# Performance work log

Measured on AMD Instinct MI355X. Metric: run time of the kernel, lower is better.

## Reference

```python
import jax, jax.numpy as jnp
import numpy as np

HEADS = 8
CHANNELS = 256
RR = 1
DH = CHANNELS // RR                 # per-head channels
ATT = HEADS * DH                    # 2048
# exact scale from the torch module
SCALE = (1.0 / np.sqrt(CHANNELS // RR)) / np.sqrt(2.0 / (CHANNELS + 3 * ATT)) * np.sqrt(2.0 / (CHANNELS + ATT))


def setup_inputs() -> dict:
    key = jax.random.key(0)
    k1, k2, k3, k4, k5 = jax.random.split(key, 5)
    x = jax.random.normal(k1, (8, CHANNELS, 32, 32), dtype=jnp.float32)
    # 1x1 conv weights stored as [out_ch, in_ch]
    w_in = jax.random.normal(k2, (3 * ATT, CHANNELS), dtype=jnp.float32) * (1.0 / np.sqrt(CHANNELS))
    b_in = jax.random.normal(k3, (3 * ATT,), dtype=jnp.float32) * 0.02
    w_out = jax.random.normal(k4, (CHANNELS, ATT), dtype=jnp.float32) * (1.0 / np.sqrt(ATT))
    b_out = jax.random.normal(k5, (CHANNELS,), dtype=jnp.float32) * 0.02
    return {"x": x, "w_in": w_in, "b_in": b_in, "w_out": w_out, "b_out": b_out}


def reference(x, w_in, b_in, w_out, b_out):
    n, c, h, w = x.shape
    L = h * w
    xf = x.reshape(n, c, L)
    # 1x1 conv in = channel-mixing matmul, then fixed scale
    scaled = (jnp.einsum('ncl,oc->nol', xf, w_in) + b_in[:, None]) * jnp.float32(SCALE)
    s = scaled.reshape(n, HEADS, 3 * DH, L)
    q, k, v = s[:, :, :DH], s[:, :, DH:2 * DH], s[:, :, 2 * DH:]   # each (n, H, DH, L)
    att = jnp.einsum('nhdl,nhdm->nhlm', q, k)                       # (n, H, L, L)
    # softmax over the FLATTENED L*L axis (global per head), as in the torch code
    att = jax.nn.softmax(att.reshape(n, HEADS, L * L), axis=2).reshape(n, HEADS, L, L)
    out = jnp.einsum('nhdl,nhlm->nhdm', v, att)                     # (n, H, DH, L)
    out = out.reshape(n, ATT, L)
    out = jnp.einsum('nal,ca->ncl', out, w_out) + b_out[:, None]
    return out.reshape(n, c, h, w)
```

## Files before the change

kernel.cpp:

```cpp
#include <hip/hip_runtime.h>
#include <hip/hip_bf16.h>


typedef __bf16 bf16x8 __attribute__((ext_vector_type(8)));
typedef __bf16 bf16x4 __attribute__((ext_vector_type(4)));
typedef float f32x4 __attribute__((ext_vector_type(4)));
typedef float f32x16 __attribute__((ext_vector_type(16)));
typedef __hip_bfloat16 bf16;

__device__ __forceinline__ void async_copy16(const void* g, void* s) {
    __builtin_amdgcn_global_load_lds(
        (const __attribute__((address_space(1))) unsigned int*)g,
        (__attribute__((address_space(3))) unsigned int*)s, 16, 0, 0);
}

__device__ __forceinline__ bf16x8 scale8(bf16x8 v, float s) {
    bf16x8 r;
#pragma unroll
    for (int e = 0; e < 8; ++e) r[e] = (__bf16)((float)v[e] * s);
    return r;
}

__global__ __launch_bounds__(256)
void gemm_nt(const bf16* __restrict__ A, const bf16* __restrict__ B, void* __restrict__ Cvoid,
             int M, int N, int K, int lda, int ldb, int ldc,
             long asn, long ash, long bsn, long bsh, long csn, long csh,
             int H, int mode, const float* __restrict__ bias, const float* __restrict__ Zp,
             float scale,
             bf16* __restrict__ outQ, bf16* __restrict__ outK, bf16* __restrict__ outV)
{
    __shared__ __align__(16) bf16 smem[17408];
    bf16* Alds = smem;
    bf16* Blds = smem + 8192;

    const int tid  = threadIdx.x;
    const int wave = tid >> 6;
    const int lane = tid & 63;
    const int z  = blockIdx.z;
    const int zn = z / H, zh = z % H;

    const bf16* Ab = A + zn * asn + zh * ash;
    const bf16* Bb = B + zn * bsn + zh * bsh;

    const long tM = (long)blockIdx.y * 128;
    const long tN = (long)blockIdx.x * 128;

    const int wr   = (wave >> 1) * 64;
    const int wc   = (wave & 1) * 64;
    const int l15  = lane & 15;
    const int quad = lane >> 4;

    f32x4 acc[4][4] = {};

    const int kiters = K >> 6;
    const bool regB = (mode == 4);

#pragma unroll
    for (int i = 0; i < 4; ++i) {
        const int flat = i * 256 + tid;
        const int row  = flat >> 3;
        const int kcs  = (flat & 7) ^ (row & 7);
        async_copy16(Ab + (tM + row) * (long)lda + kcs * 8,
                     (char*)Alds + (long)(i * 256 + wave * 64) * 16);
        if (!regB) {
            async_copy16(Bb + (tN + row) * (long)ldb + kcs * 8,
                         (char*)Blds + (long)(i * 256 + wave * 64) * 16);
        }
    }
    if (regB) {
        const float zi0 = 1.0f / Zp[zn * 8];
#pragma unroll
        for (int i = 0; i < 4; ++i) {
            const int flat = i * 256 + tid;
            const int row  = flat >> 3;
            const int kcs  = (flat & 7) ^ (row & 7);
            bf16x8 b = *(const bf16x8*)(Bb + (tN + row) * (long)ldb + kcs * 8);
            *(bf16x8*)((char*)Blds + (long)flat * 16) = scale8(b, zi0);
        }
    }

    bf16x8 pfA[4], pfB[4];
    for (int kt = 0; kt < kiters; ++kt) {
        __syncthreads();
        const bool has_next = (kt + 1 < kiters);
        float zin = 1.0f;
        if (has_next) {
            const long kof = (long)(kt + 1) * 64;
            if (regB) zin = 1.0f / Zp[zn * 8 + ((kt + 1) >> 2)];
#pragma unroll
            for (int i = 0; i < 4; ++i) {
                const int flat = i * 256 + tid;
                const int row  = flat >> 3;
                const int kcs  = (flat & 7) ^ (row & 7);
                pfA[i] = *(const bf16x8*)(Ab + (tM + row) * (long)lda + kof + kcs * 8);
                pfB[i] = *(const bf16x8*)(Bb + (tN + row) * (long)ldb + kof + kcs * 8);
            }
        }
#pragma unroll
        for (int kk = 0; kk < 2; ++kk) {
            bf16x8 af[4], bfv[4];
#pragma unroll
            for (int i = 0; i < 4; ++i) {
                const int r = wr + i * 16 + l15;
                af[i] = *(const bf16x8*)(Alds + r * 64 + ((kk * 4 + quad) ^ (r & 7)) * 8);
            }
#pragma unroll
            for (int j = 0; j < 4; ++j) {
                const int r = wc + j * 16 + l15;
                bfv[j] = *(const bf16x8*)(Blds + r * 64 + ((kk * 4 + quad) ^ (r & 7)) * 8);
            }
#pragma unroll
            for (int i = 0; i < 4; ++i)
#pragma unroll
                for (int j = 0; j < 4; ++j)
                    acc[i][j] = __builtin_amdgcn_mfma_f32_16x16x32_bf16(af[i], bfv[j], acc[i][j], 0, 0, 0);
        }
        if (has_next) {
            __builtin_amdgcn_sched_barrier(0);
            __builtin_amdgcn_s_barrier();
            __builtin_amdgcn_sched_barrier(0);
#pragma unroll
            for (int i = 0; i < 4; ++i) {
                const int flat = i * 256 + tid;
                *(bf16x8*)((char*)Alds + (long)flat * 16) = pfA[i];
                *(bf16x8*)((char*)Blds + (long)flat * 16) = regB ? scale8(pfB[i], zin) : pfB[i];
            }
        }
    }

    if (mode >= 3) {
        float* C = (float*)Cvoid + zn * csn + zh * csh;
#pragma unroll
        for (int i = 0; i < 4; ++i)
#pragma unroll
            for (int j = 0; j < 4; ++j)
#pragma unroll
                for (int r = 0; r < 4; ++r) {
                    const long row = tM + wr + i * 16 + quad * 4 + r;
                    const long col = tN + wc + j * 16 + l15;
                    C[row * (long)ldc + col] = acc[i][j][r] + bias[row];
                }
        return;
    }

    const int x    = blockIdx.x;
    const int part = x % 6;
    const int nh   = zn * 8 + x / 6;
    const int d0   = (part & 1) * 128;
    const int by   = blockIdx.y;

    __syncthreads();
    if (part < 4) {
#pragma unroll
        for (int i = 0; i < 4; ++i)
#pragma unroll
            for (int j = 0; j < 4; ++j)
#pragma unroll
                for (int r = 0; r < 4; ++r) {
                    const int row = wr + i * 16 + quad * 4 + r;
                    const int col = wc + j * 16 + l15;
                    const float v = (acc[i][j][r] + bias[tN + col]) * scale;
                    const int c32 = col >> 3;
                    const int slot = (c32 & 8) | ((c32 & 7) ^ (row & 7));
                    smem[row * 128 + slot * 8 + (col & 7)] = __float2bfloat16(v);
                }
        __syncthreads();
        bf16* dst = (part < 2) ? outQ : outK;
#pragma unroll
        for (int k = 0; k < 8; ++k) {
            const int flat = k * 256 + tid;
            const int seg  = flat >> 6, ln = flat & 63;
            const int lb   = seg >> 3, wloc = seg & 7;
            const int row  = lb * 32 + (ln & 31);
            const int c32  = wloc * 2 + (ln >> 5);
            const int slot = (c32 & 8) | ((c32 & 7) ^ (row & 7));
            const f32x4 val = *(const f32x4*)(smem + row * 128 + slot * 8);
            const long addr = ((long)(nh * 32 + by * 4 + lb) * 16 + (d0 >> 4) + wloc) * 512 + ln * 8;
            *(f32x4*)(dst + addr) = val;
        }
    } else {
#pragma unroll
        for (int i = 0; i < 4; ++i)
#pragma unroll
            for (int j = 0; j < 4; ++j)
#pragma unroll
                for (int r = 0; r < 4; ++r) {
                    const int row = wr + i * 16 + quad * 4 + r;
                    const int col = wc + j * 16 + l15;
                    const float v = (acc[i][j][r] + bias[tN + col]) * scale;
                    const int rc = row >> 3;
                    const int slotT = (rc & 8) | ((rc & 7) ^ (col & 7));
                    smem[col * 128 + slotT * 8 + (row & 7)] = __float2bfloat16(v);
                }
        __syncthreads();
#pragma unroll
        for (int k = 0; k < 8; ++k) {
            const int flat = k * 256 + tid;
            const int seg  = flat >> 6, ln = flat & 63;
            const int kwl  = seg >> 2, g2l = seg & 3;
            const int dl   = g2l * 32 + (ln & 31);
            const int lc   = kwl * 2 + (ln >> 5);
            const int slotT = (lc & 8) | ((lc & 7) ^ (dl & 7));
            const f32x4 val = *(const f32x4*)(smem + dl * 128 + slotT * 8);
            const long addr = ((long)(nh * 64 + by * 8 + kwl) * 8 + (d0 >> 5) + g2l) * 512 + ln * 8;
            *(f32x4*)(outV + addr) = val;
        }
    }
}

__global__ __launch_bounds__(256, 2)
void attn_fused(const bf16* __restrict__ Qsw, const bf16* __restrict__ Ksw,
                const bf16* __restrict__ Vsw, bf16* __restrict__ out_tt,
                float* __restrict__ Z)
{
    __shared__ __align__(16) bf16 smem[16904];
    bf16* Ps  = smem;
    float* Zs = (float*)(smem + 16896);

    const int tid  = threadIdx.x;
    const int wave = tid >> 6, lane = tid & 63;
    const int l31  = lane & 31, hw = lane >> 5;

    const int b   = blockIdx.x;
    const int xcd = b & 7, s = b >> 3;
    const int nh  = xcd * 8 + (s >> 4);
    const int mt  = s & 15;
    const int n   = nh >> 3, h = nh & 7;
    const long m0 = (long)mt * 64;

    const int wl = wave & 1, wm = wave >> 1;

    bf16x8 Kf[16];
    {
        const bf16* kb = Ksw + ((long)(nh * 32 + mt * 2 + wm) * 16) * 512 + lane * 8;
#pragma unroll
        for (int w = 0; w < 16; ++w)
            Kf[w] = *(const bf16x8*)(kb + w * 512);
    }

    f32x16 accO[2][2] = {};
    float zsum = 0.0f;

    for (int lt = 0; lt < 16; ++lt) {
        bf16x8 vf[4][2];
#pragma unroll
        for (int kw = 0; kw < 4; ++kw)
#pragma unroll
            for (int dt = 0; dt < 2; ++dt)
                vf[kw][dt] = *(const bf16x8*)(
                    Vsw + ((long)(nh * 64 + lt * 4 + kw) * 8 + wave * 2 + dt) * 512 + lane * 8);

        const bf16* qb = Qsw + ((long)(nh * 32 + lt * 2 + wl) * 16) * 512 + lane * 8;
        f32x16 a0 = {}, a1 = {};
#pragma unroll
        for (int w = 0; w < 16; w += 2) {
            const bf16x8 q0 = *(const bf16x8*)(qb + w * 512);
            a0 = __builtin_amdgcn_mfma_f32_32x32x16_bf16(q0, Kf[w], a0, 0, 0, 0);
            const bf16x8 q1 = *(const bf16x8*)(qb + (w + 1) * 512);
            a1 = __builtin_amdgcn_mfma_f32_32x32x16_bf16(q1, Kf[w + 1], a1, 0, 0, 0);
        }

#pragma unroll
        for (int g = 0; g < 4; ++g) {
            bf16x4 pk;
#pragma unroll
            for (int e = 0; e < 4; ++e) {
                const float v = __expf(a0[g * 4 + e] + a1[g * 4 + e]);
                zsum += v;
                pk[e] = (__bf16)v;
            }
            const int l  = wl * 32 + 4 * hw + 8 * g;
            const int kw = l >> 4, off = l & 15;
            *(bf16x4*)(Ps + kw * 1536 + (wm * 32 + l31) * 24 + off) = pk;
        }

        __syncthreads();

#pragma unroll
        for (int kw = 0; kw < 4; ++kw) {
            bf16x8 pf[2];
#pragma unroll
            for (int mh = 0; mh < 2; ++mh)
                pf[mh] = *(const bf16x8*)(Ps + kw * 1536 + (mh * 32 + l31) * 24 + hw * 8);
#pragma unroll
            for (int mh = 0; mh < 2; ++mh)
#pragma unroll
                for (int dt = 0; dt < 2; ++dt)
                    accO[mh][dt] = __builtin_amdgcn_mfma_f32_32x32x16_bf16(
                        pf[mh], vf[kw][dt], accO[mh][dt], 0, 0, 0);
        }
        __syncthreads();
    }

#pragma unroll
    for (int o = 32; o > 0; o >>= 1) zsum += __shfl_down(zsum, o);
    if (lane == 0) Zs[wave] = zsum;

    bf16* Cs = smem;
#pragma unroll
    for (int mh = 0; mh < 2; ++mh)
#pragma unroll
        for (int dt = 0; dt < 2; ++dt)
#pragma unroll
            for (int r = 0; r < 16; ++r) {
                const int m = mh * 32 + (r & 3) + 8 * (r >> 2) + 4 * hw;
                const int d = wave * 64 + dt * 32 + l31;
                Cs[m * 264 + d] = __float2bfloat16(accO[mh][dt][r]);
            }
    __syncthreads();
    if (tid == 0) atomicAdd(Z + nh, (Zs[0] + Zs[1]) + (Zs[2] + Zs[3]));

    bf16* Ob = out_tt + (long)n * 2097152 + m0 * 2048 + h * 256;
#pragma unroll
    for (int k = 0; k < 8; ++k) {
        const int flat = k * 256 + tid;
        const int row  = flat >> 5;
        const int c    = flat & 31;
        const f32x4 val = *(const f32x4*)((const char*)Cs + row * 528 + c * 16);
        *(f32x4*)((char*)(Ob + (long)row * 2048) + c * 16) = val;
    }
}

__global__ void prep_convert(const float* __restrict__ w_in, const float* __restrict__ w_out,
                             bf16* __restrict__ w_in_b, bf16* __restrict__ w_out_b,
                             float* __restrict__ Z)
{
    const long gid = (long)blockIdx.x * 256 + threadIdx.x;
    if (blockIdx.x == 0 && threadIdx.x < 64) Z[threadIdx.x] = 0.0f;
    const long n1 = 6144L * 256;
    const long n2 = 256L * 2048;
    const long stride = (long)gridDim.x * 256;
    for (long i = gid; i < n1; i += stride) w_in_b[i] = __float2bfloat16(w_in[i]);
    for (long i = gid; i < n2; i += stride) w_out_b[i] = __float2bfloat16(w_out[i]);
}

__global__ void prep_xt(const float* __restrict__ x, bf16* __restrict__ x_t)
{
    __shared__ float tile[64][65];
    const int b = blockIdx.x;
    const int n = blockIdx.y;
    const int ct = b & 3, lt = b >> 2;
    const int t = threadIdx.x;
    const float* xp = x + (long)n * 256 * 1024;
#pragma unroll
    for (int i = 0; i < 16; ++i) {
        const int flat = i * 256 + t;
        const int cl = flat >> 6, ll = flat & 63;
        tile[cl][ll] = xp[(long)(ct * 64 + cl) * 1024 + lt * 64 + ll];
    }
    __syncthreads();
    bf16* xo = x_t + (long)n * 1024 * 256;
#pragma unroll
    for (int i = 0; i < 16; ++i) {
        const int flat = i * 256 + t;
        const int lr = flat >> 6, cr = flat & 63;
        xo[(long)(lt * 64 + lr) * 256 + ct * 64 + cr] = __float2bfloat16(tile[cr][lr]);
    }
}

extern "C" void kernel_launch(void* const* d_in, const int* in_sizes, int n_in,
                              void* d_out, int out_size, void* d_ws, size_t ws_size,
                              hipStream_t stream)
{
    const float* x     = (const float*)d_in[0];
    const float* w_in  = (const float*)d_in[1];
    const float* b_in  = (const float*)d_in[2];
    const float* w_out = (const float*)d_in[3];
    const float* b_out = (const float*)d_in[4];
    float* out = (float*)d_out;

    const float SCALE = 0.10416666666666667f;

    char* p = (char*)d_ws;
    bf16* Qsw     = (bf16*)p;  p += 33554432;
    bf16* Ksw     = (bf16*)p;  p += 33554432;
    bf16* Vsw     = (bf16*)p;  p += 33554432;
    bf16* out_tt  = (bf16*)p;  p += 33554432;
    bf16* x_t     = (bf16*)p;  p += 4194304;
    bf16* w_in_b  = (bf16*)p;  p += 3145728;
    bf16* w_out_b = (bf16*)p;  p += 1048576;
    float* Z      = (float*)p; p += 256;

    prep_convert<<<2048, 256, 0, stream>>>(w_in, w_out, w_in_b, w_out_b, Z);
    prep_xt<<<dim3(64, 8), 256, 0, stream>>>(x, x_t);

    gemm_nt<<<dim3(48, 8, 8), 256, 0, stream>>>(
        x_t, w_in_b, nullptr,
        1024, 6144, 256, 256, 256, 0,
        1024L * 256, 0, 0, 0, 0, 0,
        1, 0, b_in, nullptr, SCALE, Qsw, Ksw, Vsw);

    attn_fused<<<1024, 256, 0, stream>>>(Qsw, Ksw, Vsw, out_tt, Z);

    gemm_nt<<<dim3(8, 2, 8), 256, 0, stream>>>(
        w_out_b, out_tt, out,
        256, 1024, 2048, 2048, 2048, 1024,
        0, 0, 1024L * 2048, 0, 256L * 1024, 0,
        1, 4, b_out, Z, 1.0f, nullptr, nullptr, nullptr);
}
```

Measured before the change: 245.8 us.

## Split-K output projection with atomics; double-buffer P and prefetch Q in attention

The output projection GEMM is split into two K halves (heads 0-3 and 4-7) across a doubled grid z-dimension. Partial sums are accumulated into the output with atomicAdd, so the output is zeroed in the prep kernel and the bias is added only by the first half. In the attention kernel, Q fragments are held in registers and prefetched for the next tile after the barrier, and the P tile in LDS is double-buffered so the second per-iteration __syncthreads can be dropped. This trades fp32 atomics and extra registers for more parallelism in the small final GEMM and fewer barriers in the attention loop.

```diff
diff --git a/kernel.cpp b/kernel.cpp
--- a/kernel.cpp
+++ b/kernel.cpp
@@ -68,7 +68,7 @@
         }
     }
     if (regB) {
-        const float zi0 = 1.0f / Zp[zn * 8];
+        const float zi0 = 1.0f / Zp[zn * 8 + zh * 4];
 #pragma unroll
         for (int i = 0; i < 4; ++i) {
             const int flat = i * 256 + tid;
@@ -86,7 +86,7 @@
         float zin = 1.0f;
         if (has_next) {
             const long kof = (long)(kt + 1) * 64;
-            if (regB) zin = 1.0f / Zp[zn * 8 + ((kt + 1) >> 2)];
+            if (regB) zin = 1.0f / Zp[zn * 8 + zh * 4 + ((kt + 1) >> 2)];
 #pragma unroll
             for (int i = 0; i < 4; ++i) {
                 const int flat = i * 256 + tid;
@@ -138,7 +138,12 @@
                 for (int r = 0; r < 4; ++r) {
                     const long row = tM + wr + i * 16 + quad * 4 + r;
                     const long col = tN + wc + j * 16 + l15;
-                    C[row * (long)ldc + col] = acc[i][j][r] + bias[row];
+                    if (mode == 4) {
+                        const float v = acc[i][j][r] + (zh == 0 ? bias[row] : 0.0f);
+                        atomicAdd(&C[row * (long)ldc + col], v);
+                    } else {
+                        C[row * (long)ldc + col] = acc[i][j][r] + bias[row];
+                    }
                 }
         return;
     }
@@ -237,6 +242,13 @@
         for (int w = 0; w < 16; ++w)
             Kf[w] = *(const bf16x8*)(kb + w * 512);
     }
+    bf16x8 Qc[16];
+    {
+        const bf16* qb = Qsw + ((long)(nh * 32 + wl) * 16) * 512 + lane * 8;
+#pragma unroll
+        for (int w = 0; w < 16; ++w)
+            Qc[w] = *(const bf16x8*)(qb + w * 512);
+    }
 
     f32x16 accO[2][2] = {};
     float zsum = 0.0f;
@@ -250,16 +262,14 @@
                 vf[kw][dt] = *(const bf16x8*)(
                     Vsw + ((long)(nh * 64 + lt * 4 + kw) * 8 + wave * 2 + dt) * 512 + lane * 8);
 
-        const bf16* qb = Qsw + ((long)(nh * 32 + lt * 2 + wl) * 16) * 512 + lane * 8;
         f32x16 a0 = {}, a1 = {};
 #pragma unroll
         for (int w = 0; w < 16; w += 2) {
-            const bf16x8 q0 = *(const bf16x8*)(qb + w * 512);
-            a0 = __builtin_amdgcn_mfma_f32_32x32x16_bf16(q0, Kf[w], a0, 0, 0, 0);
-            const bf16x8 q1 = *(const bf16x8*)(qb + (w + 1) * 512);
-            a1 = __builtin_amdgcn_mfma_f32_32x32x16_bf16(q1, Kf[w + 1], a1, 0, 0, 0);
-        }
-
+            a0 = __builtin_amdgcn_mfma_f32_32x32x16_bf16(Qc[w], Kf[w], a0, 0, 0, 0);
+            a1 = __builtin_amdgcn_mfma_f32_32x32x16_bf16(Qc[w + 1], Kf[w + 1], a1, 0, 0, 0);
+        }
+
+        bf16* Pb = Ps + (lt & 1) * 6144;
 #pragma unroll
         for (int g = 0; g < 4; ++g) {
             bf16x4 pk;
@@ -271,17 +281,24 @@
             }
             const int l  = wl * 32 + 4 * hw + 8 * g;
             const int kw = l >> 4, off = l & 15;
-            *(bf16x4*)(Ps + kw * 1536 + (wm * 32 + l31) * 24 + off) = pk;
+            *(bf16x4*)(Pb + kw * 1536 + (wm * 32 + l31) * 24 + off) = pk;
         }
 
         __syncthreads();
+
+        if (lt < 15) {
+            const bf16* qn = Qsw + ((long)(nh * 32 + (lt + 1) * 2 + wl) * 16) * 512 + lane * 8;
+#pragma unroll
+            for (int w = 0; w < 16; ++w)
+                Qc[w] = *(const bf16x8*)(qn + w * 512);
+        }
 
 #pragma unroll
         for (int kw = 0; kw < 4; ++kw) {
             bf16x8 pf[2];
 #pragma unroll
             for (int mh = 0; mh < 2; ++mh)
-                pf[mh] = *(const bf16x8*)(Ps + kw * 1536 + (mh * 32 + l31) * 24 + hw * 8);
+                pf[mh] = *(const bf16x8*)(Pb + kw * 1536 + (mh * 32 + l31) * 24 + hw * 8);
 #pragma unroll
             for (int mh = 0; mh < 2; ++mh)
 #pragma unroll
@@ -289,8 +306,9 @@
                     accO[mh][dt] = __builtin_amdgcn_mfma_f32_32x32x16_bf16(
                         pf[mh], vf[kw][dt], accO[mh][dt], 0, 0, 0);
         }
-        __syncthreads();
-    }
+    }
+
+    __syncthreads();
 
 #pragma unroll
     for (int o = 32; o > 0; o >>= 1) zsum += __shfl_down(zsum, o);
@@ -323,10 +341,12 @@
 
 __global__ void prep_convert(const float* __restrict__ w_in, const float* __restrict__ w_out,
                              bf16* __restrict__ w_in_b, bf16* __restrict__ w_out_b,
-                             float* __restrict__ Z)
+                             float* __restrict__ Z, float* __restrict__ out)
 {
     const long gid = (long)blockIdx.x * 256 + threadIdx.x;
     if (blockIdx.x == 0 && threadIdx.x < 64) Z[threadIdx.x] = 0.0f;
+    const f32x4 z4 = {0.0f, 0.0f, 0.0f, 0.0f};
+    if (gid < 524288) ((f32x4*)out)[gid] = z4;
     const long n1 = 6144L * 256;
     const long n2 = 256L * 2048;
     const long stride = (long)gridDim.x * 256;
@@ -381,7 +401,7 @@
     bf16* w_out_b = (bf16*)p;  p += 1048576;
     float* Z      = (float*)p; p += 256;
 
-    prep_convert<<<2048, 256, 0, stream>>>(w_in, w_out, w_in_b, w_out_b, Z);
+    prep_convert<<<2048, 256, 0, stream>>>(w_in, w_out, w_in_b, w_out_b, Z, out);
     prep_xt<<<dim3(64, 8), 256, 0, stream>>>(x, x_t);
 
     gemm_nt<<<dim3(48, 8, 8), 256, 0, stream>>>(
@@ -392,9 +412,9 @@
 
     attn_fused<<<1024, 256, 0, stream>>>(Qsw, Ksw, Vsw, out_tt, Z);
 
-    gemm_nt<<<dim3(8, 2, 8), 256, 0, stream>>>(
+    gemm_nt<<<dim3(8, 2, 16), 256, 0, stream>>>(
         w_out_b, out_tt, out,
-        256, 1024, 2048, 2048, 2048, 1024,
-        0, 0, 1024L * 2048, 0, 256L * 1024, 0,
-        1, 4, b_out, Z, 1.0f, nullptr, nullptr, nullptr);
-}
+        256, 1024, 1024, 2048, 2048, 1024,
+        0, 1024, 1024L * 2048, 1024, 256L * 1024, 0,
+        2, 4, b_out, Z, 1.0f, nullptr, nullptr, nullptr);
+}
```

Result: faster. 234.3 us (-4.7%).
